# Performance work log

Measured on AMD Instinct MI355X. Metric: run time of the kernel, lower is better.

Reference implementation:

```python
import jax, jax.numpy as jnp
import numpy as np

N_THETA = 180  # matches init kwarg n_theta


def setup_inputs() -> dict:
    key = jax.random.key(0)
    image = jax.random.normal(key, (2, 1, 256, 256), dtype=jnp.float32)
    return {"image": image}


def _radon_forward(image):
    # image: [B, 1, W, W]
    B, _, W, _ = image.shape
    # circle=False: pad to the diagonal so rotation never clips content
    diag = 2.0 ** 0.5 * W
    pad = int(np.ceil(diag - W))
    S = int(np.ceil(diag))                    # padded square size (363 for W=256)
    new_center = (W + pad) // 2
    pad_before = new_center - W // 2
    pad_after = pad - pad_before
    img = jnp.pad(image[:, 0], ((0, 0), (pad_before, pad_after), (pad_before, pad_after)))  # [B,S,S]

    thetas = jnp.deg2rad(jnp.linspace(0.0, 180.0, N_THETA))
    cos_a = jnp.cos(thetas)[:, None, None]    # [A,1,1]
    sin_a = jnp.sin(thetas)[:, None, None]

    # torch affine_grid(align_corners=True): base grid in [-1,1] inclusive
    base = jnp.linspace(-1.0, 1.0, S)
    y = base[:, None]                          # height index i
    x = base[None, :]                          # width index j
    # theta = [[c, s, 0], [-s, c, 0]] -> sample coords per angle, [A,S,S]
    gx = cos_a * x + sin_a * y
    gy = -sin_a * x + cos_a * y

    # grid_sample align_corners=True: pixel coord = (g+1)/2*(S-1)
    px = (gx + 1.0) * 0.5 * (S - 1)
    py = (gy + 1.0) * 0.5 * (S - 1)
    x0 = jnp.floor(px).astype(jnp.int32); x1 = x0 + 1
    y0 = jnp.floor(py).astype(jnp.int32); y1 = y0 + 1
    wx1 = px - x0; wx0 = 1.0 - wx1
    wy1 = py - y0; wy0 = 1.0 - wy1

    def fetch(yi, xi):
        # zeros padding: out-of-range taps contribute 0
        valid = ((yi >= 0) & (yi < S) & (xi >= 0) & (xi < S)).astype(img.dtype)
        yc = jnp.clip(yi, 0, S - 1)
        xc = jnp.clip(xi, 0, S - 1)
        return img[:, yc, xc] * valid[None]    # [B,A,S,S]

    sampled = (fetch(y0, x0) * (wy0 * wx0)[None]
               + fetch(y0, x1) * (wy0 * wx1)[None]
               + fetch(y1, x0) * (wy1 * wx0)[None]
               + fetch(y1, x1) * (wy1 * wx1)[None])   # [B,A,S,S]

    sino = sampled.sum(axis=2)                 # sum over height -> [B,A,S]
    # torch: stack along dim=2 then permute(0,1,3,2) -> [B,1,S,A]
    return jnp.transpose(sino, (0, 2, 1))[:, None]


def reference(image):
    return _radon_forward(image)
```

## Files before the change

kernel.cpp:

```cpp
#include <hip/hip_runtime.h>
#include <math.h>


#define SS 363
#define WW 256
#define NT 180
#define AP 9
#define QDIM (WW + 2 * AP)
#define QCNT (QDIM * QDIM)

typedef _Float16 h4 __attribute__((ext_vector_type(4)));

__global__ __launch_bounds__(256) void radon_prep(const float* __restrict__ img,
                                                  h4* __restrict__ q) {
    const int idx = blockIdx.x * 256 + threadIdx.x;
    if (idx >= 2 * QCNT) return;
    const int b   = idx / QCNT;
    const int rem = idx - b * QCNT;
    const int iy  = rem / QDIM;
    const int ix  = rem - iy * QDIM;
    const int y0 = iy - AP, x0 = ix - AP;
    const float* __restrict__ im = img + b * WW * WW;
    float v00 = 0.f, v01 = 0.f, v10 = 0.f, v11 = 0.f;
    const bool xin0 = ((unsigned)x0 < (unsigned)WW);
    const bool xin1 = ((unsigned)(x0 + 1) < (unsigned)WW);
    if ((unsigned)y0 < (unsigned)WW) {
        const float* r0 = im + y0 * WW;
        if (xin0) v00 = r0[x0];
        if (xin1) v01 = r0[x0 + 1];
    }
    if ((unsigned)(y0 + 1) < (unsigned)WW) {
        const float* r1 = im + (y0 + 1) * WW;
        if (xin0) v10 = r1[x0];
        if (xin1) v11 = r1[x0 + 1];
    }
    h4 o;
    o.x = (_Float16)v00; o.y = (_Float16)v01;
    o.z = (_Float16)v10; o.w = (_Float16)v11;
    q[idx] = o;
}

__global__ __launch_bounds__(256) void radon_main(const h4* __restrict__ q,
                                                  float* __restrict__ out) {
    const int tid = threadIdx.x;
    const int w   = tid >> 6;
    const int l   = tid & 63;
    const int cl  = l & 7;
    const int rl  = l >> 3;
    const int tile = blockIdx.x * 4 + w;
    if (tile * 8 >= SS) return;
    const int t = blockIdx.y;
    const int b = blockIdx.z;
    const int c = tile * 8 + cl;

    float sv, cv;
    sincosf((float)t * 0.017551608191455498f, &sv, &cv);
    const float x   = fmaf((float)c, 0.0055248618784530386f, -1.0f);
    const float gx0 = fmaf(cv, x, -sv);
    const float gy0 = fmaf(-sv, x, -cv);
    const float px0 = fmaf(gx0, 181.0f, 128.0f);
    const float py0 = fmaf(gy0, 181.0f, 128.0f);

    float rlo = 0.0f, rhi = 362.0f;
    if (fabsf(sv) > 1e-8f) {
        const float ra = (-1.0f - px0) / sv, rb = (256.0f - px0) / sv;
        rlo = fmaxf(rlo, fminf(ra, rb)); rhi = fminf(rhi, fmaxf(ra, rb));
    } else if (px0 <= -1.0f || px0 >= 256.0f) rhi = -2.0f;
    if (fabsf(cv) > 1e-8f) {
        const float ra = (-1.0f - py0) / cv, rb = (256.0f - py0) / cv;
        rlo = fmaxf(rlo, fminf(ra, rb)); rhi = fminf(rhi, fmaxf(ra, rb));
    } else if (py0 <= -1.0f || py0 >= 256.0f) rhi = -2.0f;
    int Rlo = max(0, (int)floorf(rlo) - 1);
    int Rhi = min(SS - 1, (int)ceilf(rhi) + 1);
    #pragma unroll
    for (int o = 1; o <= 4; o <<= 1) {
        Rlo = min(Rlo, __shfl_xor(Rlo, o, 64));
        Rhi = max(Rhi, __shfl_xor(Rhi, o, 64));
    }

    const h4* __restrict__ qb = q + b * QCNT;
    float acc = 0.0f;
    #pragma unroll 2
    for (int r = Rlo + rl; r <= Rhi; r += 8) {
        const float rf = (float)r;
        const float px = fmaf(rf, sv, px0);
        const float py = fmaf(rf, cv, py0);
        const float fx = floorf(px), fy = floorf(py);
        const float wx1 = px - fx, wy1 = py - fy;
        const float wx0 = 1.0f - wx1, wy0 = 1.0f - wy1;
        const int xi = (int)fx + AP;
        const int yi = (int)fy + AP;
        const h4 v = qb[yi * QDIM + xi];
        const float top = fmaf(wx0, (float)v.x, wx1 * (float)v.y);
        const float bot = fmaf(wx0, (float)v.z, wx1 * (float)v.w);
        acc = fmaf(wy0, top, acc);
        acc = fmaf(wy1, bot, acc);
    }
    acc += __shfl_xor(acc, 8, 64);
    acc += __shfl_xor(acc, 16, 64);
    acc += __shfl_xor(acc, 32, 64);
    if (l < 8) {
        const int cc = tile * 8 + l;
        if (cc < SS) out[(b * SS + cc) * NT + t] = acc;
    }
}

__global__ __launch_bounds__(256) void radon_fwd_fb(const float* __restrict__ img,
                                                    float* __restrict__ out) {
    const int tid = threadIdx.x;
    const int w = tid >> 6, l = tid & 63, cl = l & 7, rl = l >> 3;
    const int c0 = blockIdx.x * 8, c = c0 + cl, t = blockIdx.y, b = blockIdx.z;
    float sv, cv;
    sincosf((float)t * 0.017551608191455498f, &sv, &cv);
    const float x   = fmaf((float)c, 0.0055248618784530386f, -1.0f);
    const float px0 = fmaf(fmaf(cv, x, -sv), 181.0f, 128.0f);
    const float py0 = fmaf(fmaf(-sv, x, -cv), 181.0f, 128.0f);
    float rlo = 0.0f, rhi = 362.0f;
    if (fabsf(sv) > 1e-8f) {
        const float ra = (-1.0f - px0) / sv, rb = (256.0f - px0) / sv;
        rlo = fmaxf(rlo, fminf(ra, rb)); rhi = fminf(rhi, fmaxf(ra, rb));
    } else if (px0 <= -1.0f || px0 >= 256.0f) rhi = -2.0f;
    if (fabsf(cv) > 1e-8f) {
        const float ra = (-1.0f - py0) / cv, rb = (256.0f - py0) / cv;
        rlo = fmaxf(rlo, fminf(ra, rb)); rhi = fminf(rhi, fmaxf(ra, rb));
    } else if (py0 <= -1.0f || py0 >= 256.0f) rhi = -2.0f;
    int Rlo = max(0, (int)floorf(rlo) - 1);
    int Rhi = min(SS - 1, (int)ceilf(rhi) + 1);
    #pragma unroll
    for (int o = 1; o <= 4; o <<= 1) {
        Rlo = min(Rlo, __shfl_xor(Rlo, o, 64));
        Rhi = max(Rhi, __shfl_xor(Rhi, o, 64));
    }
    const float* __restrict__ imgb = img + b * (WW * WW);
    float acc = 0.0f;
    for (int r = Rlo + 8 * w + rl; r <= Rhi; r += 32) {
        const float rf = (float)r;
        const float px = fmaf(rf, sv, px0), py = fmaf(rf, cv, py0);
        const float fx = floorf(px), fy = floorf(py);
        float wx1 = px - fx, wy1 = py - fy;
        float wx0 = 1.0f - wx1, wy0 = 1.0f - wy1;
        const int x0 = (int)fx, y0 = (int)fy, x1 = x0 + 1, y1 = y0 + 1;
        wx0 *= ((unsigned)x0 < (unsigned)WW) ? 1.0f : 0.0f;
        wx1 *= ((unsigned)x1 < (unsigned)WW) ? 1.0f : 0.0f;
        wy0 *= ((unsigned)y0 < (unsigned)WW) ? 1.0f : 0.0f;
        wy1 *= ((unsigned)y1 < (unsigned)WW) ? 1.0f : 0.0f;
        const int xc0 = min(max(x0, 0), WW - 1), xc1 = min(max(x1, 0), WW - 1);
        const int yc0 = min(max(y0, 0), WW - 1), yc1 = min(max(y1, 0), WW - 1);
        const float* r0p = imgb + yc0 * WW;
        const float* r1p = imgb + yc1 * WW;
        const float top = fmaf(wx0, r0p[xc0], wx1 * r0p[xc1]);
        const float bot = fmaf(wx0, r1p[xc0], wx1 * r1p[xc1]);
        acc = fmaf(wy0, top, acc);
        acc = fmaf(wy1, bot, acc);
    }
    acc += __shfl_xor(acc, 8, 64);
    acc += __shfl_xor(acc, 16, 64);
    acc += __shfl_xor(acc, 32, 64);
    __shared__ float part[4][8];
    if (l < 8) part[w][l] = acc;
    __syncthreads();
    if (tid < 8) {
        const int cc = c0 + tid;
        if (cc < SS)
            out[(b * SS + cc) * NT + t] =
                part[0][tid] + part[1][tid] + part[2][tid] + part[3][tid];
    }
}

extern "C" void kernel_launch(void* const* d_in, const int* in_sizes, int n_in,
                              void* d_out, int out_size, void* d_ws, size_t ws_size,
                              hipStream_t stream) {
    (void)in_sizes; (void)n_in; (void)out_size;
    const float* img = (const float*)d_in[0];
    float* out = (float*)d_out;
    const size_t need = (size_t)2 * QCNT * sizeof(h4);
    if (ws_size >= need) {
        h4* q = (h4*)d_ws;
        const int total = 2 * QCNT;
        hipLaunchKernelGGL(radon_prep, dim3((total + 255) / 256), dim3(256), 0,
                           stream, img, q);
        const int ntile = (SS + 7) / 8;
        dim3 grid((ntile + 3) / 4, NT, 2);
        hipLaunchKernelGGL(radon_main, grid, dim3(256), 0, stream, q, out);
    } else {
        dim3 grid((SS + 7) / 8, NT, 2);
        hipLaunchKernelGGL(radon_fwd_fb, grid, dim3(256), 0, stream, img, out);
    }
}
```

Measured before the change: 82.00 us.

## Interleave both batch images into one h8 texel and process batches together

The prep kernel now packs the 2x2 neighborhoods of both batch images into a single 16-byte fp16x8 entry, and the main kernel handles both batches in one thread. Each gather is 16 bytes instead of 8, and the coordinate and weight math is shared across batches. The grid is halved, so the kernel launches half as many blocks, each doing twice the accumulation work. In exchange there is less parallelism and higher register use per thread.

```diff
diff --git a/kernel.cpp b/kernel.cpp
--- a/kernel.cpp
+++ b/kernel.cpp
@@ -9,38 +9,43 @@
 #define QDIM (WW + 2 * AP)
 #define QCNT (QDIM * QDIM)
 
-typedef _Float16 h4 __attribute__((ext_vector_type(4)));
+typedef _Float16 h8 __attribute__((ext_vector_type(8)));
 
 __global__ __launch_bounds__(256) void radon_prep(const float* __restrict__ img,
-                                                  h4* __restrict__ q) {
+                                                  h8* __restrict__ q) {
     const int idx = blockIdx.x * 256 + threadIdx.x;
-    if (idx >= 2 * QCNT) return;
-    const int b   = idx / QCNT;
-    const int rem = idx - b * QCNT;
-    const int iy  = rem / QDIM;
-    const int ix  = rem - iy * QDIM;
+    if (idx >= QCNT) return;
+    const int iy = idx / QDIM;
+    const int ix = idx - iy * QDIM;
     const int y0 = iy - AP, x0 = ix - AP;
-    const float* __restrict__ im = img + b * WW * WW;
-    float v00 = 0.f, v01 = 0.f, v10 = 0.f, v11 = 0.f;
     const bool xin0 = ((unsigned)x0 < (unsigned)WW);
     const bool xin1 = ((unsigned)(x0 + 1) < (unsigned)WW);
-    if ((unsigned)y0 < (unsigned)WW) {
-        const float* r0 = im + y0 * WW;
-        if (xin0) v00 = r0[x0];
-        if (xin1) v01 = r0[x0 + 1];
-    }
-    if ((unsigned)(y0 + 1) < (unsigned)WW) {
-        const float* r1 = im + (y0 + 1) * WW;
-        if (xin0) v10 = r1[x0];
-        if (xin1) v11 = r1[x0 + 1];
-    }
-    h4 o;
-    o.x = (_Float16)v00; o.y = (_Float16)v01;
-    o.z = (_Float16)v10; o.w = (_Float16)v11;
+    const bool yin0 = ((unsigned)y0 < (unsigned)WW);
+    const bool yin1 = ((unsigned)(y0 + 1) < (unsigned)WW);
+    h8 o;
+    #pragma unroll
+    for (int b = 0; b < 2; ++b) {
+        const float* __restrict__ im = img + b * WW * WW;
+        float v00 = 0.f, v01 = 0.f, v10 = 0.f, v11 = 0.f;
+        if (yin0) {
+            const float* r0 = im + y0 * WW;
+            if (xin0) v00 = r0[x0];
+            if (xin1) v01 = r0[x0 + 1];
+        }
+        if (yin1) {
+            const float* r1 = im + (y0 + 1) * WW;
+            if (xin0) v10 = r1[x0];
+            if (xin1) v11 = r1[x0 + 1];
+        }
+        o[4 * b + 0] = (_Float16)v00;
+        o[4 * b + 1] = (_Float16)v01;
+        o[4 * b + 2] = (_Float16)v10;
+        o[4 * b + 3] = (_Float16)v11;
+    }
     q[idx] = o;
 }
 
-__global__ __launch_bounds__(256) void radon_main(const h4* __restrict__ q,
+__global__ __launch_bounds__(256) void radon_main(const h8* __restrict__ q,
                                                   float* __restrict__ out) {
     const int tid = threadIdx.x;
     const int w   = tid >> 6;
@@ -50,7 +55,6 @@
     const int tile = blockIdx.x * 4 + w;
     if (tile * 8 >= SS) return;
     const int t = blockIdx.y;
-    const int b = blockIdx.z;
     const int c = tile * 8 + cl;
 
     float sv, cv;
@@ -78,8 +82,7 @@
         Rhi = max(Rhi, __shfl_xor(Rhi, o, 64));
     }
 
-    const h4* __restrict__ qb = q + b * QCNT;
-    float acc = 0.0f;
+    float acc0 = 0.0f, acc1 = 0.0f;
     #pragma unroll 2
     for (int r = Rlo + rl; r <= Rhi; r += 8) {
         const float rf = (float)r;
@@ -90,18 +93,28 @@
         const float wx0 = 1.0f - wx1, wy0 = 1.0f - wy1;
         const int xi = (int)fx + AP;
         const int yi = (int)fy + AP;
-        const h4 v = qb[yi * QDIM + xi];
-        const float top = fmaf(wx0, (float)v.x, wx1 * (float)v.y);
-        const float bot = fmaf(wx0, (float)v.z, wx1 * (float)v.w);
-        acc = fmaf(wy0, top, acc);
-        acc = fmaf(wy1, bot, acc);
-    }
-    acc += __shfl_xor(acc, 8, 64);
-    acc += __shfl_xor(acc, 16, 64);
-    acc += __shfl_xor(acc, 32, 64);
+        const h8 v = q[yi * QDIM + xi];
+        const float top0 = fmaf(wx0, (float)v[0], wx1 * (float)v[1]);
+        const float bot0 = fmaf(wx0, (float)v[2], wx1 * (float)v[3]);
+        acc0 = fmaf(wy0, top0, acc0);
+        acc0 = fmaf(wy1, bot0, acc0);
+        const float top1 = fmaf(wx0, (float)v[4], wx1 * (float)v[5]);
+        const float bot1 = fmaf(wx0, (float)v[6], wx1 * (float)v[7]);
+        acc1 = fmaf(wy0, top1, acc1);
+        acc1 = fmaf(wy1, bot1, acc1);
+    }
+    acc0 += __shfl_xor(acc0, 8, 64);
+    acc0 += __shfl_xor(acc0, 16, 64);
+    acc0 += __shfl_xor(acc0, 32, 64);
+    acc1 += __shfl_xor(acc1, 8, 64);
+    acc1 += __shfl_xor(acc1, 16, 64);
+    acc1 += __shfl_xor(acc1, 32, 64);
     if (l < 8) {
         const int cc = tile * 8 + l;
-        if (cc < SS) out[(b * SS + cc) * NT + t] = acc;
+        if (cc < SS) {
+            out[(0 * SS + cc) * NT + t] = acc0;
+            out[(1 * SS + cc) * NT + t] = acc1;
+        }
     }
 }
 
@@ -173,14 +186,13 @@
     (void)in_sizes; (void)n_in; (void)out_size;
     const float* img = (const float*)d_in[0];
     float* out = (float*)d_out;
-    const size_t need = (size_t)2 * QCNT * sizeof(h4);
+    const size_t need = (size_t)QCNT * sizeof(h8);
     if (ws_size >= need) {
-        h4* q = (h4*)d_ws;
-        const int total = 2 * QCNT;
-        hipLaunchKernelGGL(radon_prep, dim3((total + 255) / 256), dim3(256), 0,
+        h8* q = (h8*)d_ws;
+        hipLaunchKernelGGL(radon_prep, dim3((QCNT + 255) / 256), dim3(256), 0,
                            stream, img, q);
         const int ntile = (SS + 7) / 8;
-        dim3 grid((ntile + 3) / 4, NT, 2);
+        dim3 grid((ntile + 3) / 4, NT, 1);
         hipLaunchKernelGGL(radon_main, grid, dim3(256), 0, stream, q, out);
     } else {
         dim3 grid((SS + 7) / 8, NT, 2);
```

Measured after the change: 73.09 us. 10.9% less time.
